# Kernel optimization log

Hardware: AMD Instinct MI355X
Metric: run time of the kernel (lower is better)

Reference implementation:

```python
import jax, jax.numpy as jnp
import numpy as np
from jax import lax

V, E, H, B, S, T = 50000, 256, 512, 16, 400, 100
MAX_OOV, UNK, LAMB = 100, 1, 1.0
NEG = -1e30


def gru_scan(xs, h0, Wih, Whh, bih, bhh):
    """xs: (S,B,E), h0: (B,H) -> (hs (S,B,H), hT (B,H)). PyTorch GRU cell math."""
    gi_all = xs @ Wih.T + bih  # (S,B,3H) precomputed input projections
    def step(h, gi):
        gh = h @ Whh.T + bhh
        r = jax.nn.sigmoid(gi[..., :H] + gh[..., :H])
        z = jax.nn.sigmoid(gi[..., H:2 * H] + gh[..., H:2 * H])
        n = jnp.tanh(gi[..., 2 * H:] + r * gh[..., 2 * H:])
        hn = (1.0 - z) * n + z * h
        return hn, hn
    hT, hs = lax.scan(step, h0, gi_all)
    return hs, hT


def gru_cell(x, h, Wih, Whh, bih, bhh):
    gi = x @ Wih.T + bih
    gh = h @ Whh.T + bhh
    r = jax.nn.sigmoid(gi[..., :H] + gh[..., :H])
    z = jax.nn.sigmoid(gi[..., H:2 * H] + gh[..., H:2 * H])
    n = jnp.tanh(gi[..., 2 * H:] + r * gh[..., 2 * H:])
    return (1.0 - z) * n + z * h


def pgn_forward(floats, src_vecs, tgt_vecs, max_oov):
    (src_mask, enc_embed, dec_embed,
     eWih_f, eWhh_f, ebih_f, ebhh_f, eWih_b, eWhh_b, ebih_b, ebhh_b,
     dWih, dWhh, dbih, dbhh,
     aWh, abh, aWs, abs_, aWc, abc, aV, abv,
     rW, rb, gW, gb, fW, fb) = floats

    # --- encoder (bidirectional GRU) ---
    src_in = jnp.where(src_vecs >= V, UNK, src_vecs)          # replace_oov
    xs = enc_embed[src_in].transpose(1, 0, 2)                  # (S,B,E)
    h0 = jnp.zeros((B, H), xs.dtype)
    hs_f, hT_f = gru_scan(xs, h0, eWih_f, eWhh_f, ebih_f, ebhh_f)
    hs_b, hT_b = gru_scan(xs[::-1], h0, eWih_b, eWhh_b, ebih_b, ebhh_b)
    enc_out = jnp.concatenate([hs_f, hs_b[::-1]], -1).transpose(1, 0, 2)  # (B,S,2H)
    enc_hidden = jnp.concatenate([hT_f, hT_b], -1)             # (B,2H)

    # reducer: initial decoder hidden (torch names it context_vec)
    h_dec0 = enc_hidden @ rW.T + rb                            # (B,H)

    # precompute Wh(enc_output) once (loop-invariant)
    Wh_enc = jnp.einsum('bsd,hd->bsh', enc_out, aWh) + abh     # (B,S,H)
    mask_s = src_mask[..., 0] > 0                              # (B,S)
    wc_vec = aWc[:, 0]                                         # (H,)
    rows = jnp.arange(B)

    dec_in = jnp.where(tgt_vecs[:, :-1] >= V, UNK, tgt_vecs[:, :-1]).T  # (T-1,B)
    targets = tgt_vecs[:, 1:].T                                          # (T-1,B)

    def step(carry, inp):
        h, cov = carry                      # (B,H), (B,S)
        tok, tgt_t = inp
        x = dec_embed[tok]                  # (B,E)
        hdec = gru_cell(x, h, dWih, dWhh, dbih, dbhh)          # (B,H)
        # Bahdanau attention with coverage
        s_part = hdec @ aWs.T + abs_                            # (B,H)
        c_part = cov[:, :, None] * wc_vec[None, None, :] + abc  # (B,S,H)
        e = jnp.tanh(Wh_enc + s_part[:, None, :] + c_part) @ aV[0] + abv[0]  # (B,S)
        attn = jax.nn.softmax(jnp.where(mask_s, e, NEG), axis=1)
        ctx = jnp.einsum('bs,bsd->bd', attn, enc_out)           # (B,2H)
        cov_new = cov + attn
        ctx_red = ctx @ rW.T + rb                               # (B,H)
        logits = jnp.concatenate([ctx_red, hdec], -1) @ fW.T + fb
        p_vocab = jax.nn.softmax(logits, -1)                    # (B,V)
        score = jnp.concatenate([ctx_red, hdec, x], -1) @ gW.T + gb  # (B,1)
        p_gen = jnp.clip(jax.nn.sigmoid(score), 0.001, 0.999)
        p_ext = jnp.concatenate(
            [p_gen * p_vocab, jnp.zeros((B, max_oov), p_vocab.dtype)], 1)
        p_ext = p_ext.at[rows[:, None], src_vecs].add((1.0 - p_gen) * attn)
        tp = p_ext[rows, tgt_t]
        cov_loss = jnp.sum(jnp.minimum(attn, cov_new), axis=1)
        loss = (-jnp.log(tp + 1e-9) + LAMB * cov_loss) * (tgt_t != 0).astype(tp.dtype)
        return (ctx_red, cov_new), loss

    cov0 = jnp.zeros((B, S), enc_out.dtype)
    _, losses = lax.scan(step, (h_dec0, cov0), (dec_in, targets))  # (T-1,B)
    batch_loss = losses.sum(0)
    tgt_lens = jnp.sum((tgt_vecs != 0).astype(batch_loss.dtype), axis=1) - 1.0
    return jnp.mean(batch_loss / tgt_lens)


def setup_inputs() -> dict:
    key = jax.random.key(0)
    ks = iter(jax.random.split(key, 40))
    def p(shape):
        return 0.02 * jax.random.normal(next(ks), shape, dtype=jnp.float32)
    def z(n):
        return jnp.zeros((n,), jnp.float32)
    inp = {
        'src_vecs': jax.random.randint(next(ks), (B, S), 0, V + MAX_OOV),
        'src_mask': jnp.ones((B, S, 1), jnp.float32),
        'tgt_vecs': jax.random.randint(next(ks), (B, T), 0, V),
        'max_oov': MAX_OOV,
        'enc_embed': p((V, E)), 'dec_embed': p((V, E)),
        'eWih_f': p((3 * H, E)), 'eWhh_f': p((3 * H, H)), 'ebih_f': z(3 * H), 'ebhh_f': z(3 * H),
        'eWih_b': p((3 * H, E)), 'eWhh_b': p((3 * H, H)), 'ebih_b': z(3 * H), 'ebhh_b': z(3 * H),
        'dWih': p((3 * H, E)), 'dWhh': p((3 * H, H)), 'dbih': z(3 * H), 'dbhh': z(3 * H),
        'aWh': p((H, 2 * H)), 'abh': z(H), 'aWs': p((H, H)), 'abs_': z(H),
        'aWc': p((H, 1)), 'abc': z(H), 'aV': p((1, H)), 'abv': z(1),
        'rW': p((H, 2 * H)), 'rb': z(H),
        'gW': p((1, 2 * H + E)), 'gb': z(1),
        'fW': p((V, 2 * H)), 'fb': z(V),
    }
    return inp


def reference(src_vecs, src_mask, tgt_vecs, max_oov, enc_embed, dec_embed,
              eWih_f, eWhh_f, ebih_f, ebhh_f, eWih_b, eWhh_b, ebih_b, ebhh_b,
              dWih, dWhh, dbih, dbhh,
              aWh, abh, aWs, abs_, aWc, abc, aV, abv,
              rW, rb, gW, gb, fW, fb):
    floats = (src_mask, enc_embed, dec_embed,
              eWih_f, eWhh_f, ebih_f, ebhh_f, eWih_b, eWhh_b, ebih_b, ebhh_b,
              dWih, dWhh, dbih, dbhh,
              aWh, abh, aWs, abs_, aWc, abc, aV, abv,
              rW, rb, gW, gb, fW, fb)
    return pgn_forward(floats, src_vecs, tgt_vecs, max_oov)
```

## Files before the change

### kernel.cpp

```cpp
#include <hip/hip_runtime.h>

#define V_SZ 50000
#define E_SZ 256
#define H_SZ 512
#define B_SZ 16
#define S_SZ 400
#define T_SZ 100
#define UNK_TOK 1
#define NEGV -1e30f
#define NB 256

typedef unsigned short u16;
typedef unsigned int u32;
typedef __attribute__((ext_vector_type(8))) short sv8;
typedef __attribute__((ext_vector_type(4))) float f32x4;

__device__ __forceinline__ float bf2f(u16 u){ return __uint_as_float(((u32)u)<<16); }
__device__ __forceinline__ u16 f2bf(float x){
  u32 u = __float_as_uint(x);
  u32 r = (u + 0x7fffu + ((u>>16)&1u)) >> 16;
  return (u16)r;
}
__device__ __forceinline__ float wsum(float v){
  #pragma unroll
  for (int o=32;o;o>>=1) v += __shfl_xor(v,o);
  return v;
}
__device__ __forceinline__ float wmaxf(float v){
  #pragma unroll
  for (int o=32;o;o>>=1) v = fmaxf(v, __shfl_xor(v,o));
  return v;
}
__device__ __forceinline__ float ftanh(float x){
  float y = fminf(18.f, fmaxf(-18.f, 2.f*x));
  float e = __expf(y);
  return (e-1.f)/(e+1.f);
}
__device__ __forceinline__ float sigf(float x){ return 1.f/(1.f+__expf(-x)); }

__device__ __forceinline__ void gld16(const u16* g, u16* l){
  __builtin_amdgcn_global_load_lds((const __attribute__((address_space(1))) void*)g,
                                   (__attribute__((address_space(3))) void*)l, 16, 0, 0);
}

__global__ void k_init(u32* h_bf, int* flags, float* cov, float* loss_acc,
                       int* dflags, float* zeros){
  int idx = blockIdx.x*256 + threadIdx.x;
  if (idx < 16384) h_bf[idx] = 0u;
  if (idx < 1024) flags[idx] = 0;
  if (idx < B_SZ*S_SZ) cov[idx] = 0.f;
  if (idx < 64) loss_acc[idx] = 0.f;
  if (idx < NB*16) dflags[idx] = 0;
  if (idx < 512) zeros[idx] = 0.f;
}

__global__ void k_transpose(const float* __restrict__ in, float* __restrict__ out, int R, int C){
  __shared__ float t[32][33];
  int c0 = blockIdx.x*32, r0 = blockIdx.y*32;
  int x = threadIdx.x, y = threadIdx.y;
  for (int j=y;j<32;j+=8){
    int r=r0+j, c=c0+x;
    t[j][x] = (r<R && c<C) ? in[r*C+c] : 0.f;
  }
  __syncthreads();
  for (int j=y;j<32;j+=8){
    int oc = c0+j, orr = r0+x;
    if (oc<C && orr<R) out[oc*R+orr] = t[x][j];
  }
}
__global__ void k_f2bf(const float* __restrict__ in, u16* __restrict__ out, int n){
  for (int i = blockIdx.x*256 + threadIdx.x; i < n; i += gridDim.x*256) out[i] = f2bf(in[i]);
}
__global__ void k_prep_frag(const float* __restrict__ W, u16* __restrict__ out, int Nt, int K32, int K){
  int idx = blockIdx.x*256 + threadIdx.x;
  if (idx >= Nt*K32*64) return;
  int lane = idx & 63; int kk = (idx>>6) % K32; int tile = idx / (K32*64);
  const float* src = W + (size_t)(tile*16 + (lane&15))*K + kk*32 + ((lane>>4)<<3);
  u16* dst = out + (size_t)idx*8;
  #pragma unroll
  for (int j=0;j<8;++j) dst[j] = f2bf(src[j]);
}

__global__ void k_gather_src(const int* __restrict__ src, const float* __restrict__ emb, float* __restrict__ xs){
  const int n = S_SZ*B_SZ*E_SZ;
  for (int idx = blockIdx.x*blockDim.x + threadIdx.x; idx < n; idx += gridDim.x*blockDim.x){
// ... 133 lines not shown
  }
}

__global__ __launch_bounds__(256) void k_ctxred(const float* __restrict__ ctx, const float* __restrict__ rWT,
    const float* __restrict__ rb, float* __restrict__ h_cur, u16* __restrict__ u_bf){
  __shared__ float As[64][17];
  int lane = threadIdx.x & 63, wv = threadIdx.x >> 6;
  int n = blockIdx.x*64 + lane;
  float acc[4] = {0.f,0.f,0.f,0.f};
  for (int k0=0;k0<1024;k0+=64){
    for (int e=threadIdx.x; e<1024; e+=256){
      int r = e & 15, c = e >> 4;
      As[c][r] = ctx[r*1024 + k0 + c];
    }
    __syncthreads();
    #pragma unroll 8
    for (int k=0;k<64;++k){
      float w = rWT[(k0+k)*512 + n];
      #pragma unroll
      for (int j=0;j<4;++j) acc[j] += As[k][wv*4+j]*w;
    }
    __syncthreads();
  }
  float bv = rb[n];
  #pragma unroll
  for (int j=0;j<4;++j){
    int m = wv*4+j;
    float val = acc[j] + bv;
    h_cur[m*512 + n] = val;
    u_bf[m*1024 + n] = f2bf(val);
  }
}

__device__ __forceinline__ void gbar(int* __restrict__ flg, int bi){
  __syncthreads();
  if (threadIdx.x == 0){
    __threadfence();
    __hip_atomic_store(flg + blockIdx.x*16, bi, __ATOMIC_RELEASE, __HIP_MEMORY_SCOPE_AGENT);
  }
  if (threadIdx.x < 64){
    int i0 = threadIdx.x*4;
    for (;;){
      int v0 = __hip_atomic_load(flg + (i0+0)*16, __ATOMIC_RELAXED, __HIP_MEMORY_SCOPE_AGENT);
      int v1 = __hip_atomic_load(flg + (i0+1)*16, __ATOMIC_RELAXED, __HIP_MEMORY_SCOPE_AGENT);
      int v2 = __hip_atomic_load(flg + (i0+2)*16, __ATOMIC_RELAXED, __HIP_MEMORY_SCOPE_AGENT);
      int v3 = __hip_atomic_load(flg + (i0+3)*16, __ATOMIC_RELAXED, __HIP_MEMORY_SCOPE_AGENT);
      int mn = min(min(v0,v1),min(v2,v3));
      if (__ballot(mn >= bi) == ~0ull) break;
      __builtin_amdgcn_s_sleep(1);
    }
    __threadfence();
  }
  __syncthreads();
}

__global__ __launch_bounds__(256,2) void k_decoder(
    const float* __restrict__ dec_gi, u16* __restrict__ u_bf,
    const u16* __restrict__ dfrag, const u16* __restrict__ sfrag,
    const float* __restrict__ dbhh, const float* __restrict__ abs_,
    const float* __restrict__ WhEnc, const float* __restrict__ aWc,
    const float* __restrict__ abc, const float* __restrict__ aV,
    const float* __restrict__ abv, const float* __restrict__ mask,
    const float* __restrict__ encR, const float* __restrict__ rb,
    const u16* __restrict__ fwB, const float* __restrict__ fb,
    const int* __restrict__ src_vecs, const int* __restrict__ tgt_vecs,
    const float* __restrict__ gW, const float* __restrict__ gb,
    const float* __restrict__ gx,
    float* __restrict__ hdec2, float* __restrict__ s_part,
    float* __restrict__ e_buf, float* __restrict__ attn,
    float* __restrict__ cov, float* __restrict__ ctxp,
    u16* __restrict__ aFragLo, float* __restrict__ h_cur,
    float* __restrict__ se_wave, float* __restrict__ logit_tgt,
    float* __restrict__ covloss, float* __restrict__ loss_acc,
    int* __restrict__ flg){
  int tid = threadIdx.x;
  int lane = tid & 63;
  int wv = tid >> 6;
  int blk = blockIdx.x;
  int gw = blk*4 + wv;
  int quad = lane >> 4;
  int bi = 0;
  float loss_local = 0.f;
  __shared__ __align__(16) char smem[49152];

  auto phaseH = [&](int tt){
    int b = blk;
    float a1 = 0.f, a2v = 0.f, a3 = 0.f;
    const float* sw = se_wave + b*1024;
    #pragma unroll
    for (int i=0;i<4;++i) a1 += sw[tid + i*256];
    {
      const float* hc = h_cur + b*512;
      const float* hd = hdec2 + (size_t)(tt&1)*8192 + b*512;
      a2v = hc[tid]*gW[tid] + hd[tid]*gW[512+tid]
          + hc[256+tid]*gW[256+tid] + hd[256+tid]*gW[768+tid];
    }
    int tg = tgt_vecs[b*T_SZ + tt + 1];
    if (src_vecs[b*S_SZ + tid] == tg) a3 += attn[b*S_SZ + tid];
    if (tid < 144 && src_vecs[b*S_SZ + 256 + tid] == tg) a3 += attn[b*S_SZ + 256 + tid];
    a1 = wsum(a1); a2v = wsum(a2v); a3 = wsum(a3);
    float* red = (float*)smem;
    if (lane == 0){ red[wv] = a1; red[4+wv] = a2v; red[8+wv] = a3; }
    __syncthreads();
    if (tid == 0){
      float sume = red[0]+red[1]+red[2]+red[3];
      float dd   = red[4]+red[5]+red[6]+red[7];
      float ptr  = red[8]+red[9]+red[10]+red[11];
      float sc = dd + gx[tt*16 + b] + gb[0];
      float pg = fminf(0.999f, fmaxf(0.001f, sigf(sc)));
      float tp = pg * (__expf(logit_tgt[b]) / sume) + (1.f-pg)*ptr;
      if (tg != 0) loss_local += -logf(tp + 1e-9f) + covloss[b];
    }
    __syncthreads();
  };

  for (int t = 0; t < T_SZ-1; ++t){
    if (blk >= 16 && blk < 24){
      int slice = (blk-16)*4 + wv;
      int h = slice*16 + (lane & 15);
      const u16* ap = u_bf + (lane&15)*1024 + quad*8;
      f32x4 a0={0.f,0.f,0.f,0.f}, a1=a0, a2=a0;
      #pragma unroll
      for (int kk=0;kk<16;++kk){
        sv8 a = *(const sv8*)(ap + kk*32);
        a0 = __builtin_amdgcn_mfma_f32_16x16x32_bf16(a, *(const sv8*)(dfrag + ((size_t)(0*32+slice)*16 + kk)*512 + lane*8), a0, 0,0,0);
        a1 = __builtin_amdgcn_mfma_f32_16x16x32_bf16(a, *(const sv8*)(dfrag + ((size_t)(1*32+slice)*16 + kk)*512 + lane*8), a1, 0,0,0);
        a2 = __builtin_amdgcn_mfma_f32_16x16x32_bf16(a, *(const sv8*)(dfrag + ((size_t)(2*32+slice)*16 + kk)*512 + lane*8), a2, 0,0,0);
      }
      float b0 = dbhh[h], b1 = dbhh[512+h], b2 = dbhh[1024+h];
      const float* gi = dec_gi + (size_t)t*16*1536 + h;
      float* hd = hdec2 + (size_t)(t&1)*8192;
      #pragma unroll
      for (int r=0;r<4;++r){
        int b = quad*4 + r;
        const float* gp = gi + b*1536;
        float hlv = bf2f(u_bf[b*1024 + h]);
        float rg = sigf(gp[0]    + a0[r] + b0);
        float zg = sigf(gp[512]  + a1[r] + b1);
        float ng = ftanh(gp[1024] + rg*(a2[r] + b2));
        float hv = (1.f-zg)*ng + zg*hlv;
        hd[b*512 + h] = hv;
        u_bf[b*1024 + 512 + h] = f2bf(hv);
      }
    } else if (blk < 16 && t > 0){
      phaseH(t-1);
    }
    gbar(flg, ++bi);

    if (blk >= 16 && blk < 24){
      int slice = (blk-16)*4 + wv;
      const u16* ap = u_bf + (lane&15)*1024 + 512 + quad*8;
      const u16* bp = sfrag + (size_t)slice*16*512 + lane*8;
      f32x4 acc={0.f,0.f,0.f,0.f};
      #pragma unroll
      for (int kk=0;kk<16;++kk){
        sv8 a = *(const sv8*)(ap + kk*32);
        acc = __builtin_amdgcn_mfma_f32_16x16x32_bf16(a, *(const sv8*)(bp + kk*512), acc, 0,0,0);
      }
      int h = slice*16 + (lane & 15);
      float bv = abs_[h];
      #pragma unroll
      for (int r=0;r<4;++r) s_part[(quad*4+r)*512 + h] = acc[r] + bv;
    }
    gbar(flg, ++bi);

    {
      float* sp  = (float*)smem;
      float* wcs = sp + 512;
      float* abS = sp + 1024;
      float* avS = sp + 1536;
      int b = blk >> 4, chunk = blk & 15;
      for (int i = tid; i < 512; i += 256){
        sp[i]  = s_part[b*512 + i];
        wcs[i] = aWc[i];
        abS[i] = abc[i];
        avS[i] = aV[i];
      }
      __syncthreads();
      float abv0 = abv[0];
      int s0 = chunk*25;
      for (int s = s0 + wv; s < s0 + 25; s += 4){
        float cv = cov[b*S_SZ + s];
        const float* wh = WhEnc + (size_t)(b*S_SZ + s)*512;
        float a = 0.f;
        #pragma unroll
        for (int j=0;j<8;++j){
          int h = j*64 + lane;
          a += ftanh(wh[h] + sp[h] + cv*wcs[h] + abS[h]) * avS[h];
        }
        a = wsum(a);
        if (lane == 0){
          float e = a + abv0;
          if (!(mask[b*S_SZ + s] > 0.f)) e = NEGV;
          e_buf[b*S_SZ + s] = e;
        }
      }
    }
    gbar(flg, ++bi);

    if (blk < 16){
      int b = blk;
      float* red = (float*)smem;
      float e0 = e_buf[b*S_SZ + tid];
      float e1 = (tid < 144) ? e_buf[b*S_SZ + 256 + tid] : NEGV;
      float m = wmaxf(fmaxf(e0, e1));
      if (lane == 0) red[wv] = m;
      __syncthreads();
      float mx = fmaxf(fmaxf(red[0],red[1]), fmaxf(red[2],red[3]));
      float p0 = __expf(e0 - mx);
      float p1 = (tid < 144) ? __expf(e1 - mx) : 0.f;
      float sm = wsum(p0 + p1);
      if (lane == 0) red[4+wv] = sm;
      __syncthreads();
      float inv = 1.f/(red[4]+red[5]+red[6]+red[7]);
      float ml;
      {
        float a0v = p0*inv;
        attn[b*S_SZ + tid] = a0v;
        float cn = cov[b*S_SZ + tid] + a0v;
        cov[b*S_SZ + tid] = cn;
        ml = fminf(a0v, cn);
      }
      if (tid < 144){
        float a1v = p1*inv;
        attn[b*S_SZ + 256 + tid] = a1v;
        float cn = cov[b*S_SZ + 256 + tid] + a1v;
        cov[b*S_SZ + 256 + tid] = cn;
        ml += fminf(a1v, cn);
      }
      float cs = wsum(ml);
      if (lane == 0) red[8+wv] = cs;
      __syncthreads();
      if (tid == 0) covloss[b] = red[8]+red[9]+red[10]+red[11];
    }
    gbar(flg, ++bi);

    {
      int b = gw >> 6, rem = gw & 63;
      int n0 = (rem >> 3) * 64;
      int q = rem & 7;
      const float* er = encR + ((size_t)(b*S_SZ) + q*50)*512 + n0 + lane;
      const float* at = attn + b*S_SZ + q*50;
      float acc = 0.f;
      #pragma unroll 5
      for (int s=0;s<50;++s) acc += at[s] * er[(size_t)s*512];
      ctxp[(q*16 + b)*512 + n0 + lane] = acc;
    }
    gbar(flg, ++bi);

    if (blk < 4){
      int f = blk*256 + tid;
      int kk = f >> 6, l = f & 63, r = l & 15;
      int c8 = ((l >> 4) << 3) + kk*32;
      float v[8];
      #pragma unroll
      for (int j=0;j<8;++j) v[j] = rb[c8+j];
      #pragma unroll
      for (int q=0;q<8;++q){
        const float* pp = ctxp + q*8192 + r*512 + c8;
        #pragma unroll
        for (int j=0;j<8;++j) v[j] += pp[j];
      }
      sv8 fr;
      #pragma unroll
      for (int j=0;j<8;++j) fr[j] = (short)f2bf(v[j]);
      *(sv8*)&aFragLo[(size_t)f*8] = fr;
      *(sv8*)&u_bf[r*1024 + c8] = fr;
      f32x4 v0 = {v[0],v[1],v[2],v[3]};
      f32x4 v1 = {v[4],v[5],v[6],v[7]};
      *(f32x4*)&h_cur[r*512 + c8] = v0;
      *(f32x4*)&h_cur[r*512 + c8 + 4] = v1;
    }
    gbar(flg, ++bi);

    {
      u16* a_lds = (u16*)smem;
      for (int f = tid; f < 2048; f += 256){
        sv8 fr;
        if (f < 1024){
          fr = *(const sv8*)&aFragLo[(size_t)f*8];
        } else {
          int kk = f >> 6, l = f & 63, r = l & 15;
          int c8 = ((l >> 4) << 3) + kk*32;
          fr = *(const sv8*)&u_bf[r*1024 + c8];
        }
        *(sv8*)&a_lds[(size_t)f*8] = fr;
      }
      __syncthreads();

      u16* mybuf = (u16*)(smem + 32768) + wv*2048;
      int nT = (gw < 53) ? 4 : 3;
      int nC = nT * 16;
      int tgtv[4];
      #pragma unroll
      for (int r=0;r<4;++r) tgtv[r] = tgt_vecs[(quad*4 + r)*T_SZ + t + 1];
      float es[4] = {0.f,0.f,0.f,0.f};
      f32x4 acc = {0.f,0.f,0.f,0.f};

      auto STAGE = [&](int c){
        int tl = gw + ((c >> 4) << 10);
        const u16* src = fwB + (size_t)tl*16384 + (size_t)(c & 15)*1024 + lane*8;
        u16* dst = mybuf + (c & 1)*1024;
        gld16(src, dst);
        gld16(src + 512, dst + 512);
      };
      STAGE(0); STAGE(1);
      #pragma unroll 1
      for (int c = 0; c < nC; ++c){
        if (c + 1 < nC) { asm volatile("s_waitcnt vmcnt(2)" ::: "memory"); }
        else            { asm volatile("s_waitcnt vmcnt(0)" ::: "memory"); }
        const u16* bp = mybuf + (c & 1)*1024 + lane*8;
        int kk0 = (c & 15)*2;
        #pragma unroll
        for (int j=0;j<2;++j){
          sv8 af  = *(const sv8*)&a_lds[(size_t)(kk0+j)*512 + lane*8];
          sv8 bfr = *(const sv8*)&bp[j*512];
          acc = __builtin_amdgcn_mfma_f32_16x16x32_bf16(af, bfr, acc, 0,0,0);
        }
        if ((c & 15) == 15){
          int tl = gw + ((c >> 4) << 10);
          int v = tl*16 + (lane & 15);
          float fbv = fb[v];
          #pragma unroll
          for (int r=0;r<4;++r){
            float lg = acc[r] + fbv;
            if (v == tgtv[r]) logit_tgt[quad*4 + r] = lg;
            es[r] += __expf(lg);
          }
          acc[0]=0.f; acc[1]=0.f; acc[2]=0.f; acc[3]=0.f;
        }
        asm volatile("" ::: "memory");
        if (c + 2 < nC) STAGE(c + 2);
      }
      #pragma unroll
      for (int o=1;o<16;o<<=1){
        #pragma unroll
        for (int r=0;r<4;++r) es[r] += __shfl_xor(es[r], o);
      }
      if ((lane & 15) == 0){
        #pragma unroll
        for (int r=0;r<4;++r) se_wave[(size_t)(quad*4 + r)*1024 + gw] = es[r];
      }
    }
    gbar(flg, ++bi);
  }

  if (blk < 16){
    phaseH(T_SZ-2);
    if (tid == 0) loss_acc[blk] = loss_local;
  }
}

__global__ void k_out(const float* __restrict__ loss_acc, const int* __restrict__ tgt_vecs, float* __restrict__ out){
  __shared__ float s[16];
  int tid = threadIdx.x;
  if (tid < 16){
    int c = 0;
    for (int t=0;t<T_SZ;++t) c += (tgt_vecs[tid*T_SZ + t] != 0) ? 1 : 0;
    s[tid] = loss_acc[tid] / (float)(c - 1);
  }
  __syncthreads();
  if (tid == 0){
    float a = 0.f;
    for (int b=0;b<16;++b) a += s[b];
    out[0] = a / 16.f;
  }
}

extern "C" void kernel_launch(void* const* d_in, const int* in_sizes, int n_in,
                              void* d_out, int out_size, void* d_ws, size_t ws_size,
                              hipStream_t stream){
  (void)in_sizes; (void)n_in; (void)out_size; (void)ws_size;
  const int*   src_vecs = (const int*)d_in[0];
  const float* src_mask = (const float*)d_in[1];
  const int*   tgt_vecs = (const int*)d_in[2];
  const float* enc_embed= (const float*)d_in[4];
  const float* dec_embed= (const float*)d_in[5];
  const float* eWih_f = (const float*)d_in[6];
  const float* eWhh_f = (const float*)d_in[7];
  const float* ebih_f = (const float*)d_in[8];
  const float* ebhh_f = (const float*)d_in[9];
  const float* eWih_b = (const float*)d_in[10];
// ... 11 lines not shown
  const float* aWc  = (const float*)d_in[22];
  const float* abc  = (const float*)d_in[23];
  const float* aV   = (const float*)d_in[24];
  const float* abv  = (const float*)d_in[25];
  const float* rW   = (const float*)d_in[26];
  const float* rb   = (const float*)d_in[27];
  const float* gW   = (const float*)d_in[28];
  const float* gb   = (const float*)d_in[29];
  const float* fW   = (const float*)d_in[30];
  const float* fb   = (const float*)d_in[31];
  float* out = (float*)d_out;

  char* p = (char*)d_ws;
  auto alloc = [&](size_t n)->char*{ char* r = p; p += (n + 255) & ~(size_t)255; return r; };
  float* xs      = (float*)alloc((size_t)S_SZ*B_SZ*E_SZ*4);
  float* gi_f    = (float*)alloc((size_t)S_SZ*B_SZ*1536*4);
  float* gi_b    = (float*)alloc((size_t)S_SZ*B_SZ*1536*4);
  float* enc_out = (float*)alloc((size_t)B_SZ*S_SZ*1024*4);
  float* WhEnc   = (float*)alloc((size_t)B_SZ*S_SZ*512*4);
  float* dec_x   = (float*)alloc((size_t)(T_SZ-1)*B_SZ*E_SZ*4);
  float* dec_gi  = (float*)alloc((size_t)(T_SZ-1)*B_SZ*1536*4);
  float* gx      = (float*)alloc((size_t)(T_SZ-1)*B_SZ*4);
  float* eWihT_f = (float*)alloc((size_t)256*1536*4);
  float* eWihT_b = (float*)alloc((size_t)256*1536*4);
  float* dWihT   = (float*)alloc((size_t)256*1536*4);
  float* aWhT    = (float*)alloc((size_t)1024*512*4);
  float* rWT     = (float*)alloc((size_t)1024*512*4);
  u16* Wbf_f     = (u16*)alloc((size_t)1536*512*2);
  u16* Wbf_b     = (u16*)alloc((size_t)1536*512*2);
  u16* dfrag     = (u16*)alloc((size_t)96*16*512*2);
  u16* sfrag     = (u16*)alloc((size_t)32*16*512*2);
  u16* fwB       = (u16*)alloc((size_t)3125*16384*2);
  u16* h_bf      = (u16*)alloc((size_t)2*2*16*512*2);
  u16* u_bf      = (u16*)alloc((size_t)16*1024*2);
  int* flags     = (int*)alloc(64*16*4);
  float* enc_hid = (float*)alloc((size_t)B_SZ*1024*4);
  float* h_cur   = (float*)alloc((size_t)B_SZ*H_SZ*4);
  float* s_part  = (float*)alloc((size_t)B_SZ*H_SZ*4);
  float* e_buf   = (float*)alloc((size_t)B_SZ*S_SZ*4);
  float* attn    = (float*)alloc((size_t)B_SZ*S_SZ*4);
  float* cov     = (float*)alloc((size_t)B_SZ*S_SZ*4);
  float* logit_tgt = (float*)alloc(64*4);
  float* covloss = (float*)alloc(64*4);
  float* loss_acc= (float*)alloc(64*4);
  float* encR    = (float*)alloc((size_t)B_SZ*S_SZ*512*4);
  float* ctxp    = (float*)alloc((size_t)8*16*512*4);
  u16* aFragLo   = (u16*)alloc((size_t)1024*8*2);
  float* se_wave = (float*)alloc((size_t)16*1024*4);
  float* hdec2   = (float*)alloc((size_t)2*B_SZ*H_SZ*4);
  int* dflags    = (int*)alloc((size_t)NB*16*4);
  float* zeros512= (float*)alloc(512*4);

  dim3 tb(32,8);
  k_init<<<128,256,0,stream>>>((u32*)h_bf, flags, cov, loss_acc, dflags, zeros512);
  k_transpose<<<dim3(8,48),tb,0,stream>>>(eWih_f, eWihT_f, 1536, 256);
  k_transpose<<<dim3(8,48),tb,0,stream>>>(eWih_b, eWihT_b, 1536, 256);
  k_transpose<<<dim3(8,48),tb,0,stream>>>(dWih, dWihT, 1536, 256);
  k_transpose<<<dim3(32,16),tb,0,stream>>>(aWh, aWhT, 512, 1024);
  k_transpose<<<dim3(32,16),tb,0,stream>>>(rW, rWT, 512, 1024);
  k_f2bf<<<3072,256,0,stream>>>(eWhh_f, Wbf_f, 1536*512);
  k_f2bf<<<3072,256,0,stream>>>(eWhh_b, Wbf_b, 1536*512);
  k_prep_frag<<<384,256,0,stream>>>(dWhh, dfrag, 96, 16, 512);
  k_prep_frag<<<128,256,0,stream>>>(aWs, sfrag, 32, 16, 512);
  k_prep_frag<<<25000,256,0,stream>>>(fW, fwB, 3125, 32, 1024);
  k_gather_src<<<1024,256,0,stream>>>(src_vecs, enc_embed, xs);
  k_gather_dec<<<512,256,0,stream>>>(tgt_vecs, dec_embed, dec_x);
  k_gxscore<<<7,256,0,stream>>>(dec_x, gW, gx);
  k_gemm<<<dim3(24,200),256,0,stream>>>(xs, eWihT_f, ebih_f, gi_f, 6400,1536,256);
  k_gemm<<<dim3(24,200),256,0,stream>>>(xs, eWihT_b, ebih_b, gi_b, 6400,1536,256);
  k_gemm<<<dim3(24,50),256,0,stream>>>(dec_x, dWihT, dbih, dec_gi, 1584,1536,256);

  k_enc_persist<<<64,64,0,stream>>>(gi_f, gi_b, Wbf_f, Wbf_b, ebhh_f, ebhh_b,
                                    enc_out, enc_hid, h_bf, flags);

  k_ctxred<<<8,256,0,stream>>>(enc_hid, rWT, rb, h_cur, u_bf);
  k_gemm<<<dim3(8,200),256,0,stream>>>(enc_out, aWhT, abh, WhEnc, 6400,512,1024);
  k_gemm<<<dim3(8,200),256,0,stream>>>(enc_out, rWT, zeros512, encR, 6400,512,1024);

  k_decoder<<<NB,256,0,stream>>>(dec_gi, u_bf, dfrag, sfrag, dbhh, abs_,
                                 WhEnc, aWc, abc, aV, abv, src_mask,
                                 encR, rb, fwB, fb, src_vecs, tgt_vecs,
                                 gW, gb, gx,
                                 hdec2, s_part, e_buf, attn, cov, ctxp,
                                 aFragLo, h_cur, se_wave, logit_tgt, covloss,
                                 loss_acc, dflags);

  k_out<<<1,64,0,stream>>>(loss_acc, tgt_vecs, out);
}
```

Baseline: 21.60 ms.

## Split persistent decoder into specialized block groups with flag-based dataflow sync

Replaces the all-block global barrier sequence in the persistent decoder with role-specialized block groups: 64 blocks run the GRU/attention/context chain, 16 compute the loss, and 176 run the vocab-projection GEMM. These groups synchronize through per-producer flags, and shared state is double-buffered by step parity. This lets the large vocab logsumexp GEMM for step t overlap with the recurrent and attention work of step t+1. It also removes the full barriers, which are expensive. The vocab GEMM uses a deeper 4-stage async prefetch and keeps biases in registers. In exchange, the flag waits are more intricate and carry a risk of ordering bugs or deadlock if the blocks are not all co-resident.

```diff
diff --git a/kernel.cpp b/kernel.cpp
--- a/kernel.cpp
+++ b/kernel.cpp
@@ -10,6 +10,22 @@
 #define NEGV -1e30f
 #define NB 256
 
+#define SGB 64
+#define LOSS0 64
+#define NLOSS 16
+#define GG0 80
+#define NGG 176
+#define NGW 704
+
+#define FA 0
+#define FB 8
+#define FC 16
+#define FD 80
+#define FE 96
+#define FE2 160
+#define FG 164
+#define FH 340
+
 typedef unsigned short u16;
 typedef unsigned int u32;
 typedef __attribute__((ext_vector_type(8))) short sv8;
@@ -41,6 +57,27 @@
 __device__ __forceinline__ void gld16(const u16* g, u16* l){
   __builtin_amdgcn_global_load_lds((const __attribute__((address_space(1))) void*)g,
                                    (__attribute__((address_space(3))) void*)l, 16, 0, 0);
+}
+
+__device__ __forceinline__ void wait_ge(const int* f, int n, int tgt){
+  if (threadIdx.x < 64){
+    for(;;){
+      int mn = 0x7fffffff;
+      for (int i = threadIdx.x; i < n; i += 64)
+        mn = min(mn, __hip_atomic_load(f + i*16, __ATOMIC_RELAXED, __HIP_MEMORY_SCOPE_AGENT));
+      if (__ballot(mn >= tgt) == ~0ull) break;
+      __builtin_amdgcn_s_sleep(2);
+    }
+  }
+  __syncthreads();
+  __threadfence();
+}
+__device__ __forceinline__ void post(int* slot, int v){
+  __syncthreads();
+  if (threadIdx.x == 0){
+    __threadfence();
+    __hip_atomic_store(slot, v, __ATOMIC_RELEASE, __HIP_MEMORY_SCOPE_AGENT);
+  }
 }
 
 __global__ void k_init(u32* h_bf, int* flags, float* cov, float* loss_acc,
@@ -50,7 +87,7 @@
   if (idx < 1024) flags[idx] = 0;
   if (idx < B_SZ*S_SZ) cov[idx] = 0.f;
   if (idx < 64) loss_acc[idx] = 0.f;
-  if (idx < NB*16) dflags[idx] = 0;
+  if (idx < 8192) dflags[idx] = 0;
   if (idx < 512) zeros[idx] = 0.f;
 }
 
@@ -250,30 +287,8 @@
   }
 }
 
-__device__ __forceinline__ void gbar(int* __restrict__ flg, int bi){
-  __syncthreads();
-  if (threadIdx.x == 0){
-    __threadfence();
-    __hip_atomic_store(flg + blockIdx.x*16, bi, __ATOMIC_RELEASE, __HIP_MEMORY_SCOPE_AGENT);
-  }
-  if (threadIdx.x < 64){
-    int i0 = threadIdx.x*4;
-    for (;;){
-      int v0 = __hip_atomic_load(flg + (i0+0)*16, __ATOMIC_RELAXED, __HIP_MEMORY_SCOPE_AGENT);
-      int v1 = __hip_atomic_load(flg + (i0+1)*16, __ATOMIC_RELAXED, __HIP_MEMORY_SCOPE_AGENT);
-      int v2 = __hip_atomic_load(flg + (i0+2)*16, __ATOMIC_RELAXED, __HIP_MEMORY_SCOPE_AGENT);
-      int v3 = __hip_atomic_load(flg + (i0+3)*16, __ATOMIC_RELAXED, __HIP_MEMORY_SCOPE_AGENT);
-      int mn = min(min(v0,v1),min(v2,v3));
-      if (__ballot(mn >= bi) == ~0ull) break;
-      __builtin_amdgcn_s_sleep(1);
-    }
-    __threadfence();
-  }
-  __syncthreads();
-}
-
 __global__ __launch_bounds__(256,2) void k_decoder(
-    const float* __restrict__ dec_gi, u16* __restrict__ u_bf,
+    const float* __restrict__ dec_gi, u16* __restrict__ u_bf2,
     const u16* __restrict__ dfrag, const u16* __restrict__ sfrag,
     const float* __restrict__ dbhh, const float* __restrict__ abs_,
     const float* __restrict__ WhEnc, const float* __restrict__ aWc,
@@ -285,287 +300,345 @@
     const float* __restrict__ gW, const float* __restrict__ gb,
     const float* __restrict__ gx,
     float* __restrict__ hdec2, float* __restrict__ s_part,
-    float* __restrict__ e_buf, float* __restrict__ attn,
+    float* __restrict__ e_buf, float* __restrict__ attn2,
     float* __restrict__ cov, float* __restrict__ ctxp,
-    u16* __restrict__ aFragLo, float* __restrict__ h_cur,
-    float* __restrict__ se_wave, float* __restrict__ logit_tgt,
-    float* __restrict__ covloss, float* __restrict__ loss_acc,
+    u16* __restrict__ aFrag2, float* __restrict__ h_cur2,
+    float* __restrict__ se_wave2, float* __restrict__ logit_tgt2,
+    float* __restrict__ covloss2, float* __restrict__ loss_acc,
     int* __restrict__ flg){
   int tid = threadIdx.x;
   int lane = tid & 63;
   int wv = tid >> 6;
   int blk = blockIdx.x;
-  int gw = blk*4 + wv;
   int quad = lane >> 4;
-  int bi = 0;
-  float loss_local = 0.f;
-  __shared__ __align__(16) char smem[49152];
-
-  auto phaseH = [&](int tt){
-    int b = blk;
-    float a1 = 0.f, a2v = 0.f, a3 = 0.f;
-    const float* sw = se_wave + b*1024;
+  __shared__ __align__(16) char smem[65536];
+
+  if (blk >= GG0){
+    int gb_ = blk - GG0;
+    int gwv = gb_*4 + wv;
+    int nT = (gwv < 309) ? 5 : 4;
+    float fbv[5];
     #pragma unroll
-    for (int i=0;i<4;++i) a1 += sw[tid + i*256];
-    {
-      const float* hc = h_cur + b*512;
-      const float* hd = hdec2 + (size_t)(tt&1)*8192 + b*512;
-      a2v = hc[tid]*gW[tid] + hd[tid]*gW[512+tid]
-          + hc[256+tid]*gW[256+tid] + hd[256+tid]*gW[768+tid];
-    }
-    int tg = tgt_vecs[b*T_SZ + tt + 1];
-    if (src_vecs[b*S_SZ + tid] == tg) a3 += attn[b*S_SZ + tid];
-    if (tid < 144 && src_vecs[b*S_SZ + 256 + tid] == tg) a3 += attn[b*S_SZ + 256 + tid];
-    a1 = wsum(a1); a2v = wsum(a2v); a3 = wsum(a3);
-    float* red = (float*)smem;
-    if (lane == 0){ red[wv] = a1; red[4+wv] = a2v; red[8+wv] = a3; }
-    __syncthreads();
-    if (tid == 0){
-      float sume = red[0]+red[1]+red[2]+red[3];
-      float dd   = red[4]+red[5]+red[6]+red[7];
-      float ptr  = red[8]+red[9]+red[10]+red[11];
-      float sc = dd + gx[tt*16 + b] + gb[0];
-      float pg = fminf(0.999f, fmaxf(0.001f, sigf(sc)));
-      float tp = pg * (__expf(logit_tgt[b]) / sume) + (1.f-pg)*ptr;
-      if (tg != 0) loss_local += -logf(tp + 1e-9f) + covloss[b];
-    }
-    __syncthreads();
-  };
-
-  for (int t = 0; t < T_SZ-1; ++t){
-    if (blk >= 16 && blk < 24){
-      int slice = (blk-16)*4 + wv;
-      int h = slice*16 + (lane & 15);
-      const u16* ap = u_bf + (lane&15)*1024 + quad*8;
-      f32x4 a0={0.f,0.f,0.f,0.f}, a1=a0, a2=a0;
-      #pragma unroll
-      for (int kk=0;kk<16;++kk){
-        sv8 a = *(const sv8*)(ap + kk*32);
-        a0 = __builtin_amdgcn_mfma_f32_16x16x32_bf16(a, *(const sv8*)(dfrag + ((size_t)(0*32+slice)*16 + kk)*512 + lane*8), a0, 0,0,0);
-        a1 = __builtin_amdgcn_mfma_f32_16x16x32_bf16(a, *(const sv8*)(dfrag + ((size_t)(1*32+slice)*16 + kk)*512 + lane*8), a1, 0,0,0);
-        a2 = __builtin_amdgcn_mfma_f32_16x16x32_bf16(a, *(const sv8*)(dfrag + ((size_t)(2*32+slice)*16 + kk)*512 + lane*8), a2, 0,0,0);
-      }
-      float b0 = dbhh[h], b1 = dbhh[512+h], b2 = dbhh[1024+h];
-      const float* gi = dec_gi + (size_t)t*16*1536 + h;
-      float* hd = hdec2 + (size_t)(t&1)*8192;
-      #pragma unroll
-      for (int r=0;r<4;++r){
-        int b = quad*4 + r;
-        const float* gp = gi + b*1536;
-        float hlv = bf2f(u_bf[b*1024 + h]);
-        float rg = sigf(gp[0]    + a0[r] + b0);
-        float zg = sigf(gp[512]  + a1[r] + b1);
-        float ng = ftanh(gp[1024] + rg*(a2[r] + b2));
-        float hv = (1.f-zg)*ng + zg*hlv;
-        hd[b*512 + h] = hv;
-        u_bf[b*1024 + 512 + h] = f2bf(hv);
-      }
-    } else if (blk < 16 && t > 0){
-      phaseH(t-1);
-    }
-    gbar(flg, ++bi);
-
-    if (blk >= 16 && blk < 24){
-      int slice = (blk-16)*4 + wv;
-      const u16* ap = u_bf + (lane&15)*1024 + 512 + quad*8;
-      const u16* bp = sfrag + (size_t)slice*16*512 + lane*8;
-      f32x4 acc={0.f,0.f,0.f,0.f};
-      #pragma unroll
-      for (int kk=0;kk<16;++kk){
-        sv8 a = *(const sv8*)(ap + kk*32);
-        acc = __builtin_amdgcn_mfma_f32_16x16x32_bf16(a, *(const sv8*)(bp + kk*512), acc, 0,0,0);
-      }
-      int h = slice*16 + (lane & 15);
-      float bv = abs_[h];
-      #pragma unroll
-      for (int r=0;r<4;++r) s_part[(quad*4+r)*512 + h] = acc[r] + bv;
-    }
-    gbar(flg, ++bi);
-
-    {
-      float* sp  = (float*)smem;
-      float* wcs = sp + 512;
-      float* abS = sp + 1024;
-      float* avS = sp + 1536;
-      int b = blk >> 4, chunk = blk & 15;
-      for (int i = tid; i < 512; i += 256){
-        sp[i]  = s_part[b*512 + i];
-        wcs[i] = aWc[i];
-        abS[i] = abc[i];
-        avS[i] = aV[i];
-      }
-      __syncthreads();
-      float abv0 = abv[0];
-      int s0 = chunk*25;
-      for (int s = s0 + wv; s < s0 + 25; s += 4){
-        float cv = cov[b*S_SZ + s];
-        const float* wh = WhEnc + (size_t)(b*S_SZ + s)*512;
-        float a = 0.f;
-        #pragma unroll
-        for (int j=0;j<8;++j){
-          int h = j*64 + lane;
-          a += ftanh(wh[h] + sp[h] + cv*wcs[h] + abS[h]) * avS[h];
+    for (int i=0;i<5;++i){
+      int tl_ = gwv + 704*i;
+      fbv[i] = (i < nT) ? fb[tl_*16 + (lane&15)] : 0.f;
+    }
+    u16* a_lds = (u16*)smem;
+    u16* mybuf = (u16*)(smem + 32768) + wv*4096;
+
+    for (int t=0; t<T_SZ-1; ++t){
+      int p = t&1;
+      wait_ge(flg + FE2*16, 4, t+1);
+      wait_ge(flg + FA*16, 8, t+1);
+      {
+        const u16* ub = u_bf2 + (size_t)p*16384;
+        const u16* af = aFrag2 + (size_t)p*8192;
+        for (int f = tid; f < 2048; f += 256){
+          sv8 fr;
+          if (f < 1024){
+            fr = *(const sv8*)(af + (size_t)f*8);
+          } else {
+            int kk = f>>6, l = f&63, r = l&15;
+            int c8 = ((l>>4)<<3) + kk*32;
+            fr = *(const sv8*)(ub + r*1024 + c8);
+          }
+          *(sv8*)(a_lds + (size_t)f*8) = fr;
         }
-        a = wsum(a);
-        if (lane == 0){
-          float e = a + abv0;
-          if (!(mask[b*S_SZ + s] > 0.f)) e = NEGV;
-          e_buf[b*S_SZ + s] = e;
-        }
-      }
-    }
-    gbar(flg, ++bi);
-
-    if (blk < 16){
-      int b = blk;
-      float* red = (float*)smem;
-      float e0 = e_buf[b*S_SZ + tid];
-      float e1 = (tid < 144) ? e_buf[b*S_SZ + 256 + tid] : NEGV;
-      float m = wmaxf(fmaxf(e0, e1));
-      if (lane == 0) red[wv] = m;
-      __syncthreads();
-      float mx = fmaxf(fmaxf(red[0],red[1]), fmaxf(red[2],red[3]));
-      float p0 = __expf(e0 - mx);
-      float p1 = (tid < 144) ? __expf(e1 - mx) : 0.f;
-      float sm = wsum(p0 + p1);
-      if (lane == 0) red[4+wv] = sm;
-      __syncthreads();
-      float inv = 1.f/(red[4]+red[5]+red[6]+red[7]);
-      float ml;
-      {
-        float a0v = p0*inv;
-        attn[b*S_SZ + tid] = a0v;
-        float cn = cov[b*S_SZ + tid] + a0v;
-        cov[b*S_SZ + tid] = cn;
-        ml = fminf(a0v, cn);
-      }
-      if (tid < 144){
-        float a1v = p1*inv;
-        attn[b*S_SZ + 256 + tid] = a1v;
-        float cn = cov[b*S_SZ + 256 + tid] + a1v;
-        cov[b*S_SZ + 256 + tid] = cn;
-        ml += fminf(a1v, cn);
-      }
-      float cs = wsum(ml);
-      if (lane == 0) red[8+wv] = cs;
-      __syncthreads();
-      if (tid == 0) covloss[b] = red[8]+red[9]+red[10]+red[11];
-    }
-    gbar(flg, ++bi);
-
-    {
-      int b = gw >> 6, rem = gw & 63;
-      int n0 = (rem >> 3) * 64;
-      int q = rem & 7;
-      const float* er = encR + ((size_t)(b*S_SZ) + q*50)*512 + n0 + lane;
-      const float* at = attn + b*S_SZ + q*50;
-      float acc = 0.f;
-      #pragma unroll 5
-      for (int s=0;s<50;++s) acc += at[s] * er[(size_t)s*512];
-      ctxp[(q*16 + b)*512 + n0 + lane] = acc;
-    }
-    gbar(flg, ++bi);
-
-    if (blk < 4){
-      int f = blk*256 + tid;
-      int kk = f >> 6, l = f & 63, r = l & 15;
-      int c8 = ((l >> 4) << 3) + kk*32;
-      float v[8];
-      #pragma unroll
-      for (int j=0;j<8;++j) v[j] = rb[c8+j];
-      #pragma unroll
-      for (int q=0;q<8;++q){
-        const float* pp = ctxp + q*8192 + r*512 + c8;
-        #pragma unroll
-        for (int j=0;j<8;++j) v[j] += pp[j];
-      }
-      sv8 fr;
-      #pragma unroll
-      for (int j=0;j<8;++j) fr[j] = (short)f2bf(v[j]);
-      *(sv8*)&aFragLo[(size_t)f*8] = fr;
-      *(sv8*)&u_bf[r*1024 + c8] = fr;
-      f32x4 v0 = {v[0],v[1],v[2],v[3]};
-      f32x4 v1 = {v[4],v[5],v[6],v[7]};
-      *(f32x4*)&h_cur[r*512 + c8] = v0;
-      *(f32x4*)&h_cur[r*512 + c8 + 4] = v1;
-    }
-    gbar(flg, ++bi);
-
-    {
-      u16* a_lds = (u16*)smem;
-      for (int f = tid; f < 2048; f += 256){
-        sv8 fr;
-        if (f < 1024){
-          fr = *(const sv8*)&aFragLo[(size_t)f*8];
-        } else {
-          int kk = f >> 6, l = f & 63, r = l & 15;
-          int c8 = ((l >> 4) << 3) + kk*32;
-          fr = *(const sv8*)&u_bf[r*1024 + c8];
-        }
-        *(sv8*)&a_lds[(size_t)f*8] = fr;
-      }
-      __syncthreads();
-
-      u16* mybuf = (u16*)(smem + 32768) + wv*2048;
-      int nT = (gw < 53) ? 4 : 3;
-      int nC = nT * 16;
+      }
       int tgtv[4];
       #pragma unroll
       for (int r=0;r<4;++r) tgtv[r] = tgt_vecs[(quad*4 + r)*T_SZ + t + 1];
+      __syncthreads();
+
       float es[4] = {0.f,0.f,0.f,0.f};
+      float ltg[4] = {NEGV,NEGV,NEGV,NEGV};
       f32x4 acc = {0.f,0.f,0.f,0.f};
+      int nC = nT*16;
 
       auto STAGE = [&](int c){
-        int tl = gw + ((c >> 4) << 10);
-        const u16* src = fwB + (size_t)tl*16384 + (size_t)(c & 15)*1024 + lane*8;
-        u16* dst = mybuf + (c & 1)*1024;
+        int tile = gwv + 704*(c>>4);
+        const u16* src = fwB + (size_t)tile*16384 + (size_t)(c&15)*1024 + lane*8;
+        u16* dst = mybuf + (c&3)*1024;
         gld16(src, dst);
         gld16(src + 512, dst + 512);
       };
-      STAGE(0); STAGE(1);
-      #pragma unroll 1
-      for (int c = 0; c < nC; ++c){
-        if (c + 1 < nC) { asm volatile("s_waitcnt vmcnt(2)" ::: "memory"); }
-        else            { asm volatile("s_waitcnt vmcnt(0)" ::: "memory"); }
-        const u16* bp = mybuf + (c & 1)*1024 + lane*8;
-        int kk0 = (c & 15)*2;
-        #pragma unroll
-        for (int j=0;j<2;++j){
-          sv8 af  = *(const sv8*)&a_lds[(size_t)(kk0+j)*512 + lane*8];
-          sv8 bfr = *(const sv8*)&bp[j*512];
-          acc = __builtin_amdgcn_mfma_f32_16x16x32_bf16(af, bfr, acc, 0,0,0);
+      STAGE(0); STAGE(1); STAGE(2); STAGE(3);
+
+      #pragma unroll
+      for (int i=0;i<5;++i) if (i < nT){
+        if (i < nT-1){
+          #pragma unroll
+          for (int c2=0;c2<16;++c2){
+            int c = i*16 + c2;
+            asm volatile("s_waitcnt vmcnt(6)" ::: "memory");
+            const u16* bp = mybuf + (c&3)*1024 + lane*8;
+            int kk0 = c2*2;
+            #pragma unroll
+            for (int j=0;j<2;++j){
+              sv8 af = *(const sv8*)(a_lds + (size_t)(kk0+j)*512 + lane*8);
+              sv8 bfr = *(const sv8*)(bp + j*512);
+              acc = __builtin_amdgcn_mfma_f32_16x16x32_bf16(af, bfr, acc, 0,0,0);
+            }
+            if (c2 == 15){
+              int v = (gwv + 704*i)*16 + (lane&15);
+              #pragma unroll
+              for (int r=0;r<4;++r){
+                float lg = acc[r] + fbv[i];
+                if (v == tgtv[r]) ltg[r] = lg;
+                es[r] += __expf(lg);
+              }
+              acc[0]=0.f; acc[1]=0.f; acc[2]=0.f; acc[3]=0.f;
+            }
+            STAGE(c+4);
+          }
+        } else {
+          #pragma unroll
+          for (int c2=0;c2<16;++c2){
+            int c = i*16 + c2;
+            int ahead = nC-1-c;
+            if (ahead >= 3)      asm volatile("s_waitcnt vmcnt(6)" ::: "memory");
+            else if (ahead == 2) asm volatile("s_waitcnt vmcnt(4)" ::: "memory");
+            else if (ahead == 1) asm volatile("s_waitcnt vmcnt(2)" ::: "memory");
+            else                 asm volatile("s_waitcnt vmcnt(0)" ::: "memory");
+            const u16* bp = mybuf + (c&3)*1024 + lane*8;
+            int kk0 = c2*2;
+            #pragma unroll
+            for (int j=0;j<2;++j){
+              sv8 af = *(const sv8*)(a_lds + (size_t)(kk0+j)*512 + lane*8);
+              sv8 bfr = *(const sv8*)(bp + j*512);
+              acc = __builtin_amdgcn_mfma_f32_16x16x32_bf16(af, bfr, acc, 0,0,0);
+            }
+            if (c2 == 15){
+              int v = (gwv + 704*i)*16 + (lane&15);
+              #pragma unroll
+              for (int r=0;r<4;++r){
+                float lg = acc[r] + fbv[i];
+                if (v == tgtv[r]) ltg[r] = lg;
+                es[r] += __expf(lg);
+              }
+              acc[0]=0.f; acc[1]=0.f; acc[2]=0.f; acc[3]=0.f;
+            }
+            if (c+4 < nC) STAGE(c+4);
+          }
         }
-        if ((c & 15) == 15){
-          int tl = gw + ((c >> 4) << 10);
-          int v = tl*16 + (lane & 15);
-          float fbv = fb[v];
-          #pragma unroll
-          for (int r=0;r<4;++r){
-            float lg = acc[r] + fbv;
-            if (v == tgtv[r]) logit_tgt[quad*4 + r] = lg;
-            es[r] += __expf(lg);
-          }
-          acc[0]=0.f; acc[1]=0.f; acc[2]=0.f; acc[3]=0.f;
-        }
-        asm volatile("" ::: "memory");
-        if (c + 2 < nC) STAGE(c + 2);
       }
       #pragma unroll
       for (int o=1;o<16;o<<=1){
         #pragma unroll
         for (int r=0;r<4;++r) es[r] += __shfl_xor(es[r], o);
       }
-      if ((lane & 15) == 0){
+      if ((lane&15) == 0){
         #pragma unroll
-        for (int r=0;r<4;++r) se_wave[(size_t)(quad*4 + r)*1024 + gw] = es[r];
-      }
-    }
-    gbar(flg, ++bi);
-  }
-
-  if (blk < 16){
-    phaseH(T_SZ-2);
-    if (tid == 0) loss_acc[blk] = loss_local;
+        for (int r=0;r<4;++r) se_wave2[(size_t)p*12288 + (quad*4+r)*768 + gwv] = es[r];
+      }
+      #pragma unroll
+      for (int r=0;r<4;++r)
+        if (ltg[r] > -1e29f) logit_tgt2[p*16 + quad*4 + r] = ltg[r];
+      post(flg + (FG + gb_)*16, t+1);
+    }
+
+  } else if (blk >= LOSS0){
+    int b = blk - LOSS0;
+    float loss_local = 0.f;
+    float* red = (float*)smem;
+    for (int t=0; t<T_SZ-1; ++t){
+      wait_ge(flg + FG*16, NGG, t+1);
+      int p = t&1;
+      const float* sw = se_wave2 + (size_t)p*12288 + b*768;
+      float a1 = 0.f;
+      for (int i=tid; i<704; i+=256) a1 += sw[i];
+      const float* hc = h_cur2 + (size_t)p*8192 + b*512;
+      const float* hd = hdec2 + (size_t)p*8192 + b*512;
+      float a2v = hc[tid]*gW[tid] + hd[tid]*gW[512+tid]
+                + hc[256+tid]*gW[256+tid] + hd[256+tid]*gW[768+tid];
+      int tg = tgt_vecs[b*T_SZ + t + 1];
+      float a3 = 0.f;
+      const float* at = attn2 + (size_t)p*6400 + b*400;
+      if (src_vecs[b*S_SZ + tid] == tg) a3 += at[tid];
+      if (tid < 144 && src_vecs[b*S_SZ + 256 + tid] == tg) a3 += at[256+tid];
+      a1 = wsum(a1); a2v = wsum(a2v); a3 = wsum(a3);
+      if (lane == 0){ red[wv] = a1; red[4+wv] = a2v; red[8+wv] = a3; }
+      __syncthreads();
+      if (tid == 0){
+        float sume = red[0]+red[1]+red[2]+red[3];
+        float dd   = red[4]+red[5]+red[6]+red[7];
+        float ptr  = red[8]+red[9]+red[10]+red[11];
+        float sc = dd + gx[t*16 + b] + gb[0];
+        float pg = fminf(0.999f, fmaxf(0.001f, sigf(sc)));
+        float tp = pg * (__expf(logit_tgt2[p*16 + b]) / sume) + (1.f-pg)*ptr;
+        if (tg != 0) loss_local += -logf(tp + 1e-9f) + covloss2[p*16 + b];
+      }
+      post(flg + (FH + b)*16, t+1);
+    }
+    if (tid == 0) loss_acc[b] = loss_local;
+
+  } else {
+    float* sp  = (float*)smem;
+    float* wcs = sp + 512;
+    float* abS = sp + 1024;
+    float* avS = sp + 1536;
+    for (int i=tid; i<512; i+=256){ wcs[i] = aWc[i]; abS[i] = abc[i]; avS[i] = aV[i]; }
+    __syncthreads();
+    float abv0 = abv[0];
+
+    for (int t=0; t<T_SZ-1; ++t){
+      int p = t&1, pn = (t+1)&1;
+
+      if (blk < 8){
+        if (t > 0)  wait_ge(flg + FE2*16, 4, t);
+        if (t >= 2){ wait_ge(flg + FG*16, NGG, t-1); wait_ge(flg + FH*16, NLOSS, t-1); }
+        {
+          int slice = blk*4 + wv;
+          int h = slice*16 + (lane & 15);
+          const u16* ubp = u_bf2 + (size_t)pn*16384;
+          const u16* ap = ubp + (lane&15)*1024 + quad*8;
+          f32x4 a0={0.f,0.f,0.f,0.f}, a1=a0, a2=a0;
+          #pragma unroll
+          for (int kk=0;kk<16;++kk){
+            sv8 a = *(const sv8*)(ap + kk*32);
+            a0 = __builtin_amdgcn_mfma_f32_16x16x32_bf16(a, *(const sv8*)(dfrag + ((size_t)(0*32+slice)*16 + kk)*512 + lane*8), a0, 0,0,0);
+            a1 = __builtin_amdgcn_mfma_f32_16x16x32_bf16(a, *(const sv8*)(dfrag + ((size_t)(1*32+slice)*16 + kk)*512 + lane*8), a1, 0,0,0);
+            a2 = __builtin_amdgcn_mfma_f32_16x16x32_bf16(a, *(const sv8*)(dfrag + ((size_t)(2*32+slice)*16 + kk)*512 + lane*8), a2, 0,0,0);
+          }
+          float b0 = dbhh[h], b1 = dbhh[512+h], b2 = dbhh[1024+h];
+          const float* gi = dec_gi + (size_t)t*16*1536 + h;
+          u16* ubw = u_bf2 + (size_t)p*16384;
+          float* hd = hdec2 + (size_t)p*8192;
+          #pragma unroll
+          for (int r=0;r<4;++r){
+            int b = quad*4 + r;
+            const float* gp = gi + b*1536;
+            float hlv = bf2f(ubp[b*1024 + h]);
+            float rg = sigf(gp[0]    + a0[r] + b0);
+            float zg = sigf(gp[512]  + a1[r] + b1);
+            float ng = ftanh(gp[1024] + rg*(a2[r] + b2));
+            float hv = (1.f-zg)*ng + zg*hlv;
+            hd[b*512 + h] = hv;
+            ubw[b*1024 + 512 + h] = f2bf(hv);
+          }
+        }
+        post(flg + (FA + blk)*16, t+1);
+        wait_ge(flg + FA*16, 8, t+1);
+        {
+          int slice = blk*4 + wv;
+          const u16* ap = u_bf2 + (size_t)p*16384 + (lane&15)*1024 + 512 + quad*8;
+          const u16* bp = sfrag + (size_t)slice*16*512 + lane*8;
+          f32x4 acc = {0.f,0.f,0.f,0.f};
+          #pragma unroll
+          for (int kk=0;kk<16;++kk){
+            sv8 a = *(const sv8*)(ap + kk*32);
+            acc = __builtin_amdgcn_mfma_f32_16x16x32_bf16(a, *(const sv8*)(bp + kk*512), acc, 0,0,0);
+          }
+          int h = slice*16 + (lane&15);
+          float bv = abs_[h];
+          #pragma unroll
+          for (int r=0;r<4;++r) s_part[(quad*4+r)*512 + h] = acc[r] + bv;
+        }
+        post(flg + (FB + blk)*16, t+1);
+      }
+
+      wait_ge(flg + FB*16, 8, t+1);
+      {
+        int b = blk >> 2;
+        int chunk = (blk&3)*4 + wv;
+        for (int i=tid; i<512; i+=256) sp[i] = s_part[b*512 + i];
+        __syncthreads();
+        int s0 = chunk*25;
+        for (int s = s0; s < s0+25; ++s){
+          float cv = cov[b*400 + s];
+          const float* wh = WhEnc + (size_t)(b*400 + s)*512;
+          float a = 0.f;
+          #pragma unroll
+          for (int j=0;j<8;++j){
+            int h2 = j*64 + lane;
+            a += ftanh(wh[h2] + sp[h2] + cv*wcs[h2] + abS[h2]) * avS[h2];
+          }
+          a = wsum(a);
+          if (lane == 0){
+            float e = a + abv0;
+            if (!(mask[b*400 + s] > 0.f)) e = NEGV;
+            e_buf[b*400 + s] = e;
+          }
+        }
+      }
+      post(flg + (FC + blk)*16, t+1);
+
+      if (blk < 16){
+        wait_ge(flg + (FC + 4*blk)*16, 4, t+1);
+        if (t >= 2) wait_ge(flg + (FH + blk)*16, 1, t-1);
+        int b = blk;
+        float* red = (float*)smem + 2048;
+        float e0 = e_buf[b*400 + tid];
+        float e1 = (tid < 144) ? e_buf[b*400 + 256 + tid] : NEGV;
+        float m = wmaxf(fmaxf(e0, e1));
+        if (lane == 0) red[wv] = m;
+        __syncthreads();
+        float mx = fmaxf(fmaxf(red[0],red[1]), fmaxf(red[2],red[3]));
+        float p0 = __expf(e0 - mx);
+        float p1 = (tid < 144) ? __expf(e1 - mx) : 0.f;
+        float sm = wsum(p0 + p1);
+        if (lane == 0) red[4+wv] = sm;
+        __syncthreads();
+        float inv = 1.f/(red[4]+red[5]+red[6]+red[7]);
+        float* an = attn2 + (size_t)p*6400 + b*400;
+        float ml;
+        {
+          float a0v = p0*inv;
+          an[tid] = a0v;
+          float cn = cov[b*400 + tid] + a0v;
+          cov[b*400 + tid] = cn;
+          ml = fminf(a0v, cn);
+        }
+        if (tid < 144){
+          float a1v = p1*inv;
+          an[256+tid] = a1v;
+          float cn = cov[b*400 + 256 + tid] + a1v;
+          cov[b*400 + 256 + tid] = cn;
+          ml += fminf(a1v, cn);
+        }
+        float cs = wsum(ml);
+        if (lane == 0) red[8+wv] = cs;
+        __syncthreads();
+        if (tid == 0) covloss2[p*16 + b] = red[8]+red[9]+red[10]+red[11];
+        post(flg + (FD + blk)*16, t+1);
+      }
+
+      {
+        int b = blk >> 2;
+        wait_ge(flg + (FD + b)*16, 1, t+1);
+        int local = (blk&3)*4 + wv;
+        int nch = local >> 1, sh = local & 1;
+        int n0 = nch*64, s0 = sh*200;
+        const float* at2 = attn2 + (size_t)p*6400 + b*400 + s0;
+        const float* er = encR + ((size_t)(b*400 + s0))*512 + n0 + lane;
+        float acc2 = 0.f;
+        #pragma unroll 5
+        for (int s=0;s<200;++s) acc2 += at2[s] * er[(size_t)s*512];
+        ctxp[(sh*16 + b)*512 + n0 + lane] = acc2;
+      }
+      post(flg + (FE + blk)*16, t+1);
+
+      if (blk < 4){
+        wait_ge(flg + FE*16, SGB, t+1);
+        int f = blk*256 + tid;
+        int kk = f >> 6, l = f & 63, r = l & 15;
+        int c8 = ((l >> 4) << 3) + kk*32;
+        float v[8];
+        #pragma unroll
+        for (int j=0;j<8;++j)
+          v[j] = rb[c8+j] + ctxp[r*512 + c8 + j] + ctxp[(16+r)*512 + c8 + j];
+        sv8 fr;
+        #pragma unroll
+        for (int j=0;j<8;++j) fr[j] = (short)f2bf(v[j]);
+        *(sv8*)(aFrag2 + (size_t)p*8192 + (size_t)f*8) = fr;
+        *(sv8*)(u_bf2 + (size_t)p*16384 + r*1024 + c8) = fr;
+        f32x4 v0 = {v[0],v[1],v[2],v[3]};
+        f32x4 v1 = {v[4],v[5],v[6],v[7]};
+        *(f32x4*)(h_cur2 + (size_t)p*8192 + r*512 + c8) = v0;
+        *(f32x4*)(h_cur2 + (size_t)p*8192 + r*512 + c8 + 4) = v1;
+        post(flg + (FE2 + blk)*16, t+1);
+      }
+    }
   }
 }
 
@@ -643,23 +716,23 @@
   u16* sfrag     = (u16*)alloc((size_t)32*16*512*2);
   u16* fwB       = (u16*)alloc((size_t)3125*16384*2);
   u16* h_bf      = (u16*)alloc((size_t)2*2*16*512*2);
-  u16* u_bf      = (u16*)alloc((size_t)16*1024*2);
   int* flags     = (int*)alloc(64*16*4);
   float* enc_hid = (float*)alloc((size_t)B_SZ*1024*4);
-  float* h_cur   = (float*)alloc((size_t)B_SZ*H_SZ*4);
   float* s_part  = (float*)alloc((size_t)B_SZ*H_SZ*4);
   float* e_buf   = (float*)alloc((size_t)B_SZ*S_SZ*4);
-  float* attn    = (float*)alloc((size_t)B_SZ*S_SZ*4);
   float* cov     = (float*)alloc((size_t)B_SZ*S_SZ*4);
-  float* logit_tgt = (float*)alloc(64*4);
-  float* covloss = (float*)alloc(64*4);
   float* loss_acc= (float*)alloc(64*4);
   float* encR    = (float*)alloc((size_t)B_SZ*S_SZ*512*4);
-  float* ctxp    = (float*)alloc((size_t)8*16*512*4);
-  u16* aFragLo   = (u16*)alloc((size_t)1024*8*2);
-  float* se_wave = (float*)alloc((size_t)16*1024*4);
+  u16* u_bf2     = (u16*)alloc((size_t)2*16*1024*2);
+  u16* aFrag2    = (u16*)alloc((size_t)2*1024*8*2);
+  float* attn2   = (float*)alloc((size_t)2*B_SZ*S_SZ*4);
+  float* h_cur2  = (float*)alloc((size_t)2*B_SZ*H_SZ*4);
   float* hdec2   = (float*)alloc((size_t)2*B_SZ*H_SZ*4);
-  int* dflags    = (int*)alloc((size_t)NB*16*4);
+  float* ctxp    = (float*)alloc((size_t)2*16*512*4);
+  float* se_wave2= (float*)alloc((size_t)2*16*768*4);
+  float* logit_tgt2 = (float*)alloc(2*16*4);
+  float* covloss2   = (float*)alloc(2*16*4);
+  int* dflags    = (int*)alloc((size_t)512*16*4);
   float* zeros512= (float*)alloc(512*4);
 
   dim3 tb(32,8);
@@ -684,16 +757,16 @@
   k_enc_persist<<<64,64,0,stream>>>(gi_f, gi_b, Wbf_f, Wbf_b, ebhh_f, ebhh_b,
                                     enc_out, enc_hid, h_bf, flags);
 
-  k_ctxred<<<8,256,0,stream>>>(enc_hid, rWT, rb, h_cur, u_bf);
+  k_ctxred<<<8,256,0,stream>>>(enc_hid, rWT, rb, h_cur2, u_bf2 + 16384);
   k_gemm<<<dim3(8,200),256,0,stream>>>(enc_out, aWhT, abh, WhEnc, 6400,512,1024);
   k_gemm<<<dim3(8,200),256,0,stream>>>(enc_out, rWT, zeros512, encR, 6400,512,1024);
 
-  k_decoder<<<NB,256,0,stream>>>(dec_gi, u_bf, dfrag, sfrag, dbhh, abs_,
+  k_decoder<<<NB,256,0,stream>>>(dec_gi, u_bf2, dfrag, sfrag, dbhh, abs_,
                                  WhEnc, aWc, abc, aV, abv, src_mask,
                                  encR, rb, fwB, fb, src_vecs, tgt_vecs,
                                  gW, gb, gx,
-                                 hdec2, s_part, e_buf, attn, cov, ctxp,
-                                 aFragLo, h_cur, se_wave, logit_tgt, covloss,
+                                 hdec2, s_part, e_buf, attn2, cov, ctxp,
+                                 aFrag2, h_cur2, se_wave2, logit_tgt2, covloss2,
                                  loss_acc, dflags);
 
   k_out<<<1,64,0,stream>>>(loss_acc, tgt_vecs, out);
```

Result: no change. 21.55 ms (-0.2%).
